# Performance work log

Hardware: AMD Instinct MI355X
Metric: run time of the kernel (lower is better)

## Reference

```python
import jax, jax.numpy as jnp
import numpy as np

N = 100000
NEG_SLOPE = 0.2
EPS = 1e-16


def _gatconv(h_in, src, dst, W, a_src, a_dst, b):
    # h_in: [N, Fin]; src/dst: [E_tot] (self-loops included); W: [Fin, Fout]
    h = h_in @ W                                  # [N, Fout]
    alpha_s = h @ a_src                           # [N]
    alpha_d = h @ a_dst                           # [N]
    e = alpha_s[src] + alpha_d[dst]               # [E_tot]
    e = jnp.where(e > 0, e, NEG_SLOPE * e)        # leaky_relu
    m = jax.ops.segment_max(e, dst, num_segments=N)
    e = jnp.exp(e - m[dst])
    s = jax.ops.segment_sum(e, dst, num_segments=N)
    alpha = e / (s[dst] + EPS)                    # segment softmax over in-edges of each dst
    out = jax.ops.segment_sum(alpha[:, None] * h[src], dst, num_segments=N)
    return out + b


def setup_inputs() -> dict:
    key = jax.random.key(0)
    ks = jax.random.split(key, 10)
    Fin, Fh, Fo = 64, 64, 40
    E = 1600000
    x = jax.random.normal(ks[0], (N, Fin), dtype=jnp.float32)
    edge_index = jax.random.randint(ks[1], (2, E), 0, N, dtype=jnp.int64)
    g = 1.0 / np.sqrt(Fin)
    W1 = jax.random.uniform(ks[2], (Fin, Fh), jnp.float32, -g, g)
    a_src1 = jax.random.uniform(ks[3], (Fh,), jnp.float32, -g, g)
    a_dst1 = jax.random.uniform(ks[4], (Fh,), jnp.float32, -g, g)
    b1 = jnp.zeros((Fh,), jnp.float32)
    g2 = 1.0 / np.sqrt(Fh)
    W2 = jax.random.uniform(ks[5], (Fh, Fo), jnp.float32, -g2, g2)
    a_src2 = jax.random.uniform(ks[6], (Fo,), jnp.float32, -g2, g2)
    a_dst2 = jax.random.uniform(ks[7], (Fo,), jnp.float32, -g2, g2)
    b2 = jnp.zeros((Fo,), jnp.float32)
    return {"x": x, "edge_index": edge_index, "W1": W1, "a_src1": a_src1,
            "a_dst1": a_dst1, "b1": b1, "W2": W2, "a_src2": a_src2,
            "a_dst2": a_dst2, "b2": b2}


def reference(x, edge_index, W1, a_src1, a_dst1, b1, W2, a_src2, a_dst2, b2):
    # add self loops (PyG GATConv default)
    loops = jnp.arange(N, dtype=edge_index.dtype)
    src = jnp.concatenate([edge_index[0], loops])
    dst = jnp.concatenate([edge_index[1], loops])
    h = _gatconv(x, src, dst, W1, a_src1, a_dst1, b1)
    h = jax.nn.relu(h)  # dropout p=0 / eval -> no-op
    h = _gatconv(h, src, dst, W2, a_src2, a_dst2, b2)
    return jax.nn.log_softmax(h, axis=-1)
```

## Files before the change

kernel.cpp:

```cpp
#include <hip/hip_runtime.h>
#include <math.h>

#ifndef NEG_SLOPE
#define NEG_SLOPE 0.2f
#endif

#define BUCK_BITS 9
#define BUCK_SIZE 512
#define BUCK_CAP  12288
#define PA_ILP    8
#define SMAX      0x1FFFF

__device__ __forceinline__ void get_edge(const void* ei, int is64, int e, int E,
                                         int& s, int& d) {
    if (e >= E) { s = e - E; d = s; return; }
    if (is64) {
        const long long* p = (const long long*)ei;
        s = (int)p[e];
        d = (int)p[(long long)E + e];
    } else {
        const int* p = (const int*)ei;
        s = p[e];
        d = p[E + e];
    }
}

__device__ __forceinline__ unsigned f2bf1(float x) {
    unsigned u = __float_as_uint(x);
    return (u + 0x7fffu + ((u >> 16) & 1u)) >> 16;
}

__global__ __launch_bounds__(256) void bin_gemm1(
    const void* __restrict__ ei, int E, int Etot, int binB, int gemmB, int period,
    int* __restrict__ fill, unsigned* __restrict__ pairs,
    const float* __restrict__ x, const float* __restrict__ W1,
    const float* __restrict__ avs, const float* __restrict__ avd,
    unsigned short* __restrict__ Hb, float* __restrict__ asn,
    float* __restrict__ adn, int N) {
    __shared__ __align__(16) char smem[16896];
    const int t = threadIdx.x;
    const int bi = blockIdx.x;
    const bool isBin = (bi % period) == 0;

    if (isBin) {
        const int bb = bi / period;
        int* cnt   = (int*)smem;
        int* goff  = cnt + 256;
        int* sflag = goff + 256;
        if (t < 64) {
            const int* p = (const int*)ei;
            int bad = 0;
            for (int j = 0; j < 4; ++j) bad |= (p[2 * (t * 4 + j) + 1] != 0);
            unsigned long long m = __ballot(bad);
            if (t == 0) *sflag = (m == 0ull) ? 1 : 0;
        }
        cnt[t] = 0;
        __syncthreads();
        const int is64 = *sflag;
        const int base = bb * (256 * PA_ILP) + t;
        int s[PA_ILP], d[PA_ILP], r[PA_ILP];
        bool ok[PA_ILP];
#pragma unroll
        for (int u = 0; u < PA_ILP; ++u) {
            int e = base + u * 256;
            ok[u] = (e < Etot);
            s[u] = d[u] = 0;
            if (ok[u]) get_edge(ei, is64, e, E, s[u], d[u]);
        }
#pragma unroll
        for (int u = 0; u < PA_ILP; ++u)
            if (ok[u]) r[u] = atomicAdd(&cnt[d[u] >> BUCK_BITS], 1);
        __syncthreads();
        if (cnt[t] > 0) goff[t] = atomicAdd(&fill[t], cnt[t]);
        __syncthreads();
#pragma unroll
        for (int u = 0; u < PA_ILP; ++u) {
            if (ok[u]) {
                int b = d[u] >> BUCK_BITS;
                int idx = goff[b] + r[u];
                if (idx < BUCK_CAP)
                    pairs[(size_t)b * BUCK_CAP + idx] =
                        (unsigned)s[u] | ((unsigned)(d[u] & (BUCK_SIZE - 1)) << 17);
            }
        }
    } else {
        const int gi = bi - bi / period - 1;
        if (gi >= gemmB) return;
        constexpr int K = 64, F = 64, TPR = 4, R = 64, C = 16;
        float* sW  = (float*)smem;
        float* sas = sW + K * F;
        float* sad = sas + F;

        for (int i = t; i < K * F / 4; i += 256)
            ((float4*)sW)[i] = ((const float4*)W1)[i];
        if (t < F) { sas[t] = avs[t]; sad[t] = avd[t]; }
        __syncthreads();

        const int base = gi * R;
        const int r  = t / TPR;
        const int f0 = (t % TPR) * C;
        const int row = base + r;
        float acc[C];
#pragma unroll
        for (int j = 0; j < C; ++j) acc[j] = 0.f;
        if (row < N) {
            const float4* xr = (const float4*)(x + (size_t)row * K);
#pragma unroll
            for (int c4 = 0; c4 < 16; ++c4) {
                float4 a = xr[c4];
                const float* w0 = &sW[(c4 * 4 + 0) * F + f0];
                const float* w1 = &sW[(c4 * 4 + 1) * F + f0];
                const float* w2 = &sW[(c4 * 4 + 2) * F + f0];
                const float* w3 = &sW[(c4 * 4 + 3) * F + f0];
#pragma unroll
                for (int j = 0; j < C; ++j)
                    acc[j] += a.x * w0[j] + a.y * w1[j] + a.z * w2[j] + a.w * w3[j];
            }
        }
        float ps = 0.f, pd = 0.f;
#pragma unroll
        for (int j = 0; j < C; ++j) { ps += acc[j] * sas[f0 + j]; pd += acc[j] * sad[f0 + j]; }
#pragma unroll
        for (int off = 1; off < TPR; off <<= 1) {
            ps += __shfl_xor(ps, off);
            pd += __shfl_xor(pd, off);
        }
        if (row < N) {
            if ((t % TPR) == 0) { asn[row] = ps; adn[row] = pd; }
            unsigned* hp = (unsigned*)(Hb + (size_t)row * F + f0);
#pragma unroll
            for (int j = 0; j < C / 2; ++j)
                hp[j] = f2bf1(acc[2 * j]) | (f2bf1(acc[2 * j + 1]) << 16);
        }
    }
}

__global__ __launch_bounds__(256) void bucket_csr(
    const unsigned* __restrict__ pairs, const int* __restrict__ fill,
    int* __restrict__ row_ptr, int* __restrict__ csr_src, int N, int nbuck) {
    __shared__ int cnt[BUCK_SIZE];
    __shared__ int offs[BUCK_SIZE];
    __shared__ int sbase[256];
    __shared__ int stot;
    const int t = threadIdx.x;
    if (t < 64) {
        int v[4];
        int loc = 0;
#pragma unroll
        for (int i = 0; i < 4; ++i) {
            int idx = t * 4 + i;
            v[i] = (idx < nbuck) ? fill[idx] : 0;
            loc += v[i];
        }
        int x = loc;
        for (int off = 1; off < 64; off <<= 1) {
            int y = __shfl_up(x, off);
            if (t >= off) x += y;
        }
        int run = x - loc;
#pragma unroll
        for (int i = 0; i < 4; ++i) {
            int idx = t * 4 + i;
            if (idx < 256) sbase[idx] = run;
            run += v[i];
        }
        if (t == 63) stot = x;
    }
    cnt[t] = 0; cnt[t + 256] = 0;
    __syncthreads();

    const int b = blockIdx.x;
    const int gb = sbase[b];
    int m = fill[b];
    if (m > BUCK_CAP) m = BUCK_CAP;
    if (b == 0 && t == 0) row_ptr[N] = stot;
    const unsigned* bp = pairs + (size_t)b * BUCK_CAP;

    int i = t;
    for (; i + 768 < m; i += 1024) {
        unsigned p0 = bp[i], p1 = bp[i + 256], p2 = bp[i + 512], p3 = bp[i + 768];
        atomicAdd(&cnt[p0 >> 17], 1);
        atomicAdd(&cnt[p1 >> 17], 1);
        atomicAdd(&cnt[p2 >> 17], 1);
        atomicAdd(&cnt[p3 >> 17], 1);
    }
    for (; i < m; i += 256) atomicAdd(&cnt[bp[i] >> 17], 1);
    __syncthreads();

    if (t < 64) {
        int v[8];
        int loc = 0;
#pragma unroll
        for (int j = 0; j < 8; ++j) { v[j] = cnt[t * 8 + j]; loc += v[j]; }
        int x = loc;
        for (int off = 1; off < 64; off <<= 1) {
            int y = __shfl_up(x, off);
            if (t >= off) x += y;
        }
        int run = x - loc;
#pragma unroll
        for (int j = 0; j < 8; ++j) { offs[t * 8 + j] = gb + run; run += v[j]; }
    }
    __syncthreads();

    const int base_d = b << BUCK_BITS;
    for (int k = t; k < BUCK_SIZE; k += 256) {
        int d = base_d + k;
        if (d < N) row_ptr[d] = offs[k];
    }
    __syncthreads();

    i = t;
    for (; i + 768 < m; i += 1024) {
        unsigned p0 = bp[i], p1 = bp[i + 256], p2 = bp[i + 512], p3 = bp[i + 768];
        csr_src[atomicAdd(&offs[p0 >> 17], 1)] = p0 & SMAX;
        csr_src[atomicAdd(&offs[p1 >> 17], 1)] = p1 & SMAX;
        csr_src[atomicAdd(&offs[p2 >> 17], 1)] = p2 & SMAX;
        csr_src[atomicAdd(&offs[p3 >> 17], 1)] = p3 & SMAX;
    }
    for (; i < m; i += 256) {
        unsigned p = bp[i];
        csr_src[atomicAdd(&offs[p >> 17], 1)] = p & SMAX;
    }
}

__device__ __forceinline__ void bf16x8_fma(uint4 hv, float w, float* acc) {
    const unsigned* u = (const unsigned*)&hv;
#pragma unroll
    for (int i = 0; i < 4; ++i) {
        float lo = __uint_as_float(u[i] << 16);
        float hi = __uint_as_float(u[i] & 0xffff0000u);
        acc[2 * i]     += w * lo;
        acc[2 * i + 1] += w * hi;
    }
}

__global__ __launch_bounds__(256) void agg1_gemm2(
    const int* __restrict__ row_ptr, const int* __restrict__ csr_src,
    const float* __restrict__ asn1, const float* __restrict__ adn1,
    const unsigned short* __restrict__ Hb, const float* __restrict__ b1,
    const float* __restrict__ W2, const float* __restrict__ a_s2,
    const float* __restrict__ a_d2, unsigned short* __restrict__ Hb2,
    float* __restrict__ asn2, float* __restrict__ adn2, int N) {
    __shared__ float sW2[64 * 40];
    __shared__ float sa2[40], sd2[40], sb1[64];
    __shared__ __align__(16) float rowbuf[16][68];
    const int t = threadIdx.x;
    for (int i = t; i < 640; i += 256) ((float4*)sW2)[i] = ((const float4*)W2)[i];
    if (t < 40) { sa2[t] = a_s2[t]; sd2[t] = a_d2[t]; }
    if (t >= 64 && t < 128) sb1[t - 64] = b1[t - 64];
    __syncthreads();

    const int lane    = t & 63;
    const int sub     = lane & 15;
    const int half    = sub >> 3;
    const int q       = sub & 7;
    const int grpbase = lane & 48;
    const int slot    = t >> 4;
    const int node    = blockIdx.x * 16 + slot;
    const bool valid  = node < N;
    const int nd      = valid ? node : N - 1;

    const int r0 = row_ptr[nd], r1 = row_ptr[nd + 1];
    const float add = adn1[nd];

    float acc[8];
#pragma unroll
    for (int i = 0; i < 8; ++i) acc[i] = 0.f;
    float Ssum = 0.f;

    for (int base = r0; base < r1; base += 16) {
        int cnt = r1 - base;
        if (cnt > 16) cnt = 16;
        int s = 0;
        float w = 0.f;
        if (sub < cnt) {
            s = csr_src[base + sub];
            float v = asn1[s] + add;
            v = v > 0.f ? v : NEG_SLOPE * v;
            w = __expf(v);
        }
        Ssum += w;
        for (int j = 0; j < cnt; j += 8) {
            int se[4]; float we[4]; uint4 hv[4];
#pragma unroll
            for (int k = 0; k < 4; ++k) {
                int e = j + 2 * k + half;
                int src_lane = grpbase | (e & 15);
                se[k] = __shfl(s, src_lane);
                float wk = __shfl(w, src_lane);
                we[k] = (e < cnt) ? wk : 0.f;
            }
#pragma unroll
            for (int k = 0; k < 4; ++k)
                hv[k] = *(const uint4*)(Hb + (size_t)se[k] * 64 + q * 8);
#pragma unroll
            for (int k = 0; k < 4; ++k) bf16x8_fma(hv[k], we[k], acc);
        }
    }
#pragma unroll
    for (int i = 0; i < 8; ++i) acc[i] += __shfl_xor(acc[i], 8);
#pragma unroll
    for (int off = 1; off < 16; off <<= 1) Ssum += __shfl_xor(Ssum, off);
    const float inv = 1.f / (Ssum + 1e-16f);

    if (half == 0) {
#pragma unroll
        for (int i = 0; i < 8; ++i)
            rowbuf[slot][q * 8 + i] = fmaxf(acc[i] * inv + sb1[q * 8 + i], 0.f);
    }

    const bool actT = sub < 10;
    const int f4 = 4 * (actT ? sub : 9);
    float h2[4] = {0.f, 0.f, 0.f, 0.f};
    const float4* rb4 = (const float4*)rowbuf[slot];
#pragma unroll 2
    for (int k4 = 0; k4 < 16; ++k4) {
        float4 a = rb4[k4];
        float av[4] = {a.x, a.y, a.z, a.w};
#pragma unroll
        for (int kk = 0; kk < 4; ++kk) {
            float4 wv = *(const float4*)&sW2[(k4 * 4 + kk) * 40 + f4];
            h2[0] += av[kk] * wv.x;
            h2[1] += av[kk] * wv.y;
            h2[2] += av[kk] * wv.z;
            h2[3] += av[kk] * wv.w;
        }
    }
    float ps = 0.f, pd = 0.f;
    if (actT) {
#pragma unroll
        for (int c = 0; c < 4; ++c) {
            ps += h2[c] * sa2[f4 + c];
            pd += h2[c] * sd2[f4 + c];
        }
    }
#pragma unroll
    for (int off = 1; off < 16; off <<= 1) {
        ps += __shfl_xor(ps, off);
        pd += __shfl_xor(pd, off);
    }
    if (valid && actT) {
        uint2 pk;
        pk.x = f2bf1(h2[0]) | (f2bf1(h2[1]) << 16);
        pk.y = f2bf1(h2[2]) | (f2bf1(h2[3]) << 16);
        *(uint2*)(Hb2 + (size_t)node * 40 + f4) = pk;
    }
    if (valid && sub == 0) { asn2[node] = ps; adn2[node] = pd; }
}

__global__ __launch_bounds__(256) void agg2_lsm(
    const int* __restrict__ row_ptr, const int* __restrict__ csr_src,
    const float* __restrict__ asn, const float* __restrict__ adn,
    const unsigned short* __restrict__ Hb, const float* __restrict__ bias,
    float* __restrict__ out, int N) {
    const int lane    = threadIdx.x & 63;
    const int sub     = lane & 15;
    const int esl     = sub / 5;
    const int q5      = sub - esl * 5;
    const bool act    = sub < 15;
    const int qc      = act ? q5 : 0;
    const float qmask = act ? 1.f : 0.f;
    const int grpbase = lane & 48;
    const int node    = blockIdx.x * 16 + (threadIdx.x >> 4);
    const bool valid  = node < N;
    const int nd      = valid ? node : N - 1;

    const int r0 = row_ptr[nd], r1 = row_ptr[nd + 1];
    const float add = adn[nd];

    float acc[8];
#pragma unroll
    for (int i = 0; i < 8; ++i) acc[i] = 0.f;
    float Ssum = 0.f;

    for (int base = r0; base < r1; base += 16) {
        int cnt = r1 - base;
        if (cnt > 16) cnt = 16;
        int s = 0;
        float w = 0.f;
        if (sub < cnt) {
            s = csr_src[base + sub];
            float v = asn[s] + add;
            v = v > 0.f ? v : NEG_SLOPE * v;
            w = __expf(v);
        }
        Ssum += w;
        for (int j = 0; j < cnt; j += 12) {
            int se[4]; float we[4]; uint4 hv[4];
#pragma unroll
            for (int k = 0; k < 4; ++k) {
                int e  = j + 3 * k + esl;
                int el = (e < 16) ? e : 15;
                se[k] = __shfl(s, grpbase | el);
                float wk = __shfl(w, grpbase | el) * qmask;
                we[k] = (e < cnt) ? wk : 0.f;
            }
#pragma unroll
            for (int k = 0; k < 4; ++k)
                hv[k] = *(const uint4*)(Hb + (size_t)se[k] * 40 + qc * 8);
#pragma unroll
            for (int k = 0; k < 4; ++k) bf16x8_fma(hv[k], we[k], acc);
        }
    }
#pragma unroll
    for (int i = 0; i < 8; ++i) {
        float a1 = __shfl(acc[i], grpbase + q5 + 5);
        float a2 = __shfl(acc[i], grpbase + q5 + 10);
        acc[i] += a1 + a2;
    }
#pragma unroll
    for (int off = 1; off < 16; off <<= 1) Ssum += __shfl_xor(Ssum, off);
    const float inv = 1.f / (Ssum + 1e-16f);
    const bool owner = act && (esl == 0);

    float val[8];
#pragma unroll
    for (int i = 0; i < 8; ++i) val[i] = acc[i] * inv + bias[qc * 8 + i];
    float mx = -3.0e38f;
    if (owner) {
#pragma unroll
        for (int i = 0; i < 8; ++i) mx = fmaxf(mx, val[i]);
    }
#pragma unroll
    for (int off = 1; off <= 8; off <<= 1) mx = fmaxf(mx, __shfl_xor(mx, off));
    float sm = 0.f;
    if (owner) {
#pragma unroll
        for (int i = 0; i < 8; ++i) sm += __expf(val[i] - mx);
    }
#pragma unroll
    for (int off = 1; off <= 8; off <<= 1) sm += __shfl_xor(sm, off);
    float ls = logf(sm) + mx;
    if (valid && owner) {
        float* op = out + (size_t)node * 40 + q5 * 8;
        ((float4*)op)[0] = make_float4(val[0] - ls, val[1] - ls, val[2] - ls, val[3] - ls);
        ((float4*)op)[1] = make_float4(val[4] - ls, val[5] - ls, val[6] - ls, val[7] - ls);
    }
}

extern "C" void kernel_launch(void* const* d_in, const int* in_sizes, int n_in,
                              void* d_out, int out_size, void* d_ws, size_t ws_size,
                              hipStream_t stream) {
    const float* x   = (const float*)d_in[0];
    const void*  ei  = d_in[1];
    const float* W1  = (const float*)d_in[2];
    const float* as1 = (const float*)d_in[3];
    const float* ad1 = (const float*)d_in[4];
    const float* b1  = (const float*)d_in[5];
    const float* W2  = (const float*)d_in[6];
    const float* as2 = (const float*)d_in[7];
    const float* ad2 = (const float*)d_in[8];
    const float* b2  = (const float*)d_in[9];
    float* out = (float*)d_out;

    const int N     = in_sizes[0] / 64;
    const int E     = in_sizes[1] / 2;
    const int Etot  = E + N;
    const int nbuck = (N + BUCK_SIZE - 1) >> BUCK_BITS;

    float* ws = (float*)d_ws;
    unsigned short* hb  = (unsigned short*)ws;  ws += (size_t)N * 32;
    unsigned short* hb2 = (unsigned short*)ws;  ws += (size_t)N * 20;
    float* asn1 = ws;              ws += N;
    float* adn1 = ws;              ws += N;
    float* asn2 = ws;              ws += N;
    float* adn2 = ws;              ws += N;
    int* row_ptr = (int*)ws;       ws += N + 1;
    int* csr_src = (int*)ws;       ws += Etot;
    int* fill   = (int*)ws;        ws += 256;
    unsigned* pairs = (unsigned*)ws;  ws += (size_t)256 * BUCK_CAP;

    const int binB   = (Etot + 256 * PA_ILP - 1) / (256 * PA_ILP);
    const int gemmB  = (N + 63) / 64;
    const int period = gemmB / binB + 2;
    const int grid1  = binB * period;
    const int AGG_B  = (N + 15) / 16;

    hipMemsetAsync(fill, 0, 256 * sizeof(int), stream);
    bin_gemm1<<<grid1, 256, 0, stream>>>(
        ei, E, Etot, binB, gemmB, period, fill, pairs,
        x, W1, as1, ad1, hb, asn1, adn1, N);
    bucket_csr<<<nbuck, 256, 0, stream>>>(pairs, fill, row_ptr, csr_src, N, nbuck);
    agg1_gemm2<<<AGG_B, 256, 0, stream>>>(
        row_ptr, csr_src, asn1, adn1, hb, b1, W2, as2, ad2, hb2, asn2, adn2, N);
    agg2_lsm<<<AGG_B, 256, 0, stream>>>(
        row_ptr, csr_src, asn2, adn2, hb2, b2, out, N);
}
```

Measured before the change: 223.8 us.

## Compute layer-2 projection in agg1 kernel with bf16 MFMA instead of scalar FMA

The 16-node x 64 by 64x40 projection fused into the layer-1 aggregation kernel now runs on MFMA 16x16x32 bf16 instructions using three waves, one per 16-column tile. W2 is held in registers as bf16 fragments and the activated rows are staged in shared memory as bf16. Attention logits are reduced with shuffles and combined through shared memory. This removes the scalar FMA loop and the W2 shared-memory load, but adds extra block barriers, bf16 rounding of the layer-1 activations before the projection, and per-element 2-byte stores of Hb2 instead of packed 8-byte stores.

Result: no change. 222.1 us (-0.7%).

```diff
diff --git a/kernel.cpp b/kernel.cpp
--- a/kernel.cpp
+++ b/kernel.cpp
@@ -10,6 +10,9 @@
 #define BUCK_CAP  12288
 #define PA_ILP    8
 #define SMAX      0x1FFFF
+
+typedef __attribute__((ext_vector_type(8))) short bhalf8;
+typedef __attribute__((ext_vector_type(4))) float f32x4;
 
 __device__ __forceinline__ void get_edge(const void* ei, int is64, int e, int E,
                                          int& s, int& d) {
@@ -242,16 +245,38 @@
     const float* __restrict__ W2, const float* __restrict__ a_s2,
     const float* __restrict__ a_d2, unsigned short* __restrict__ Hb2,
     float* __restrict__ asn2, float* __restrict__ adn2, int N) {
-    __shared__ float sW2[64 * 40];
-    __shared__ float sa2[40], sd2[40], sb1[64];
-    __shared__ __align__(16) float rowbuf[16][68];
+    __shared__ __align__(16) unsigned short rb16[16][72];
+    __shared__ float sa2[48], sd2[48], sb1[64];
+    __shared__ float sps3[3][16], spd3[3][16];
     const int t = threadIdx.x;
-    for (int i = t; i < 640; i += 256) ((float4*)sW2)[i] = ((const float4*)W2)[i];
-    if (t < 40) { sa2[t] = a_s2[t]; sd2[t] = a_d2[t]; }
+    if (t < 48) {
+        sa2[t] = (t < 40) ? a_s2[t] : 0.f;
+        sd2[t] = (t < 40) ? a_d2[t] : 0.f;
+    }
     if (t >= 64 && t < 128) sb1[t - 64] = b1[t - 64];
-    __syncthreads();
-
-    const int lane    = t & 63;
+
+    const int lane = t & 63;
+    const int wv   = t >> 6;
+    const int tile = (wv < 3) ? wv : 0;
+
+    bhalf8 bfr[2];
+    {
+        const int col = tile * 16 + (lane & 15);
+        const int kb  = (lane >> 4) * 8;
+        const bool cv = col < 40;
+#pragma unroll
+        for (int ks = 0; ks < 2; ++ks) {
+            bhalf8 bb;
+#pragma unroll
+            for (int j = 0; j < 8; ++j) {
+                float v = cv ? W2[(size_t)(kb + 32 * ks + j) * 40 + col] : 0.f;
+                bb[j] = (short)f2bf1(v);
+            }
+            bfr[ks] = bb;
+        }
+    }
+    __syncthreads();
+
     const int sub     = lane & 15;
     const int half    = sub >> 3;
     const int q       = sub & 7;
@@ -305,48 +330,52 @@
     const float inv = 1.f / (Ssum + 1e-16f);
 
     if (half == 0) {
-#pragma unroll
-        for (int i = 0; i < 8; ++i)
-            rowbuf[slot][q * 8 + i] = fmaxf(acc[i] * inv + sb1[q * 8 + i], 0.f);
-    }
-
-    const bool actT = sub < 10;
-    const int f4 = 4 * (actT ? sub : 9);
-    float h2[4] = {0.f, 0.f, 0.f, 0.f};
-    const float4* rb4 = (const float4*)rowbuf[slot];
-#pragma unroll 2
-    for (int k4 = 0; k4 < 16; ++k4) {
-        float4 a = rb4[k4];
-        float av[4] = {a.x, a.y, a.z, a.w};
-#pragma unroll
-        for (int kk = 0; kk < 4; ++kk) {
-            float4 wv = *(const float4*)&sW2[(k4 * 4 + kk) * 40 + f4];
-            h2[0] += av[kk] * wv.x;
-            h2[1] += av[kk] * wv.y;
-            h2[2] += av[kk] * wv.z;
-            h2[3] += av[kk] * wv.w;
-        }
-    }
-    float ps = 0.f, pd = 0.f;
-    if (actT) {
-#pragma unroll
-        for (int c = 0; c < 4; ++c) {
-            ps += h2[c] * sa2[f4 + c];
-            pd += h2[c] * sd2[f4 + c];
-        }
-    }
-#pragma unroll
-    for (int off = 1; off < 16; off <<= 1) {
-        ps += __shfl_xor(ps, off);
-        pd += __shfl_xor(pd, off);
-    }
-    if (valid && actT) {
-        uint2 pk;
-        pk.x = f2bf1(h2[0]) | (f2bf1(h2[1]) << 16);
-        pk.y = f2bf1(h2[2]) | (f2bf1(h2[3]) << 16);
-        *(uint2*)(Hb2 + (size_t)node * 40 + f4) = pk;
-    }
-    if (valid && sub == 0) { asn2[node] = ps; adn2[node] = pd; }
+        unsigned pk[4];
+#pragma unroll
+        for (int i = 0; i < 4; ++i) {
+            float v0 = fmaxf(acc[2 * i]     * inv + sb1[q * 8 + 2 * i],     0.f);
+            float v1 = fmaxf(acc[2 * i + 1] * inv + sb1[q * 8 + 2 * i + 1], 0.f);
+            pk[i] = f2bf1(v0) | (f2bf1(v1) << 16);
+        }
+        *(uint4*)&rb16[slot][q * 8] = make_uint4(pk[0], pk[1], pk[2], pk[3]);
+    }
+    __syncthreads();
+
+    if (wv < 3) {
+        f32x4 dacc = {0.f, 0.f, 0.f, 0.f};
+#pragma unroll
+        for (int ks = 0; ks < 2; ++ks) {
+            bhalf8 afr = *(const bhalf8*)&rb16[lane & 15][(lane >> 4) * 8 + 32 * ks];
+            dacc = __builtin_amdgcn_mfma_f32_16x16x32_bf16(afr, bfr[ks], dacc, 0, 0, 0);
+        }
+        const int f   = tile * 16 + (lane & 15);
+        const float saf = sa2[f];
+        const float sdf = sd2[f];
+        float psl = 0.f, pdl = 0.f;
+#pragma unroll
+        for (int i = 0; i < 4; ++i) {
+            psl = dacc[i] * saf;
+            pdl = dacc[i] * sdf;
+#pragma unroll
+            for (int off = 1; off < 16; off <<= 1) {
+                psl += __shfl_xor(psl, off);
+                pdl += __shfl_xor(pdl, off);
+            }
+            const int m  = (lane >> 4) * 4 + i;
+            if ((lane & 15) == 0) { sps3[tile][m] = psl; spd3[tile][m] = pdl; }
+            const int nn = blockIdx.x * 16 + m;
+            if (f < 40 && nn < N)
+                Hb2[(size_t)nn * 40 + f] = (unsigned short)f2bf1(dacc[i]);
+        }
+    }
+    __syncthreads();
+    if (t < 16) {
+        const int nn = blockIdx.x * 16 + t;
+        if (nn < N) {
+            asn2[nn] = sps3[0][t] + sps3[1][t] + sps3[2][t];
+            adn2[nn] = spd3[0][t] + spd3[1][t] + spd3[2][t];
+        }
+    }
 }
 
 __global__ __launch_bounds__(256) void agg2_lsm(
```
